# Kernel optimization log

Measured on AMD Instinct MI355X. Metric: run time of the kernel, lower is better.

## Reference

```python
import jax, jax.numpy as jnp
import numpy as np

N = 4096        # number_of_users
IN = 1000       # in_size (items)
H1, H2 = 2048, 1024
EMB = 512
HEADS = 8
OUT = 1000


def setup_inputs() -> dict:
    key = jax.random.key(0)
    ks = iter(jax.random.split(key, 32))
    def lin(i, o):
        return jax.random.normal(next(ks), (i, o), jnp.float32) * (1.0 / np.sqrt(i))
    inp = {"batch": jax.random.normal(next(ks), (N, IN), jnp.float32)}
    for p in ("q", "k", "v"):
        inp[p + "_w1"] = lin(IN, H1); inp[p + "_b1"] = jnp.zeros((H1,), jnp.float32)
        inp[p + "_w2"] = lin(H1, H2); inp[p + "_b2"] = jnp.zeros((H2,), jnp.float32)
        inp[p + "_w3"] = lin(H2, EMB); inp[p + "_b3"] = jnp.zeros((EMB,), jnp.float32)
    inp["wo_w"] = lin(EMB, OUT)
    inp["wo_b"] = jnp.zeros((OUT,), jnp.float32)
    return inp


def _mlp(x, w1, b1, w2, b2, w3, b3):
    h = jax.nn.relu(x @ w1 + b1)
    h = jax.nn.relu(h @ w2 + b2)
    return h @ w3 + b3


def _split_heads(x):
    # [N, EMB] -> [HEADS, N, depth]
    return x.reshape(N, HEADS, EMB // HEADS).transpose(1, 0, 2)


def reference(batch,
              q_w1, q_b1, q_w2, q_b2, q_w3, q_b3,
              k_w1, k_b1, k_w2, k_b2, k_w3, k_b3,
              v_w1, v_b1, v_w2, v_b2, v_w3, v_b3,
              wo_w, wo_b):
    q = _mlp(batch, q_w1, q_b1, q_w2, q_b2, q_w3, q_b3)
    k = _mlp(batch, k_w1, k_b1, k_w2, k_b2, k_w3, k_b3)
    v = _mlp(batch, v_w1, v_b1, v_w2, v_b2, v_w3, v_b3)
    qh = jax.nn.relu(_split_heads(q))
    kh = jax.nn.relu(_split_heads(k))
    vh = _split_heads(v)
    depth = EMB // HEADS
    # ReLU-normalized attention (no softmax): scores / row-sum
    scores = jnp.einsum('hnd,hmd->hnm', qh, kh) / jnp.sqrt(jnp.float32(depth))
    denom = jnp.sum(scores, axis=-1, keepdims=True) + 1e-8
    weights = scores / denom
    att = jnp.einsum('hnm,hmd->hnd', weights, vh)   # [H, N, depth]
    att = att.transpose(1, 0, 2).reshape(N, EMB)
    return att @ wo_w + wo_b
```

## Files before the change

### kernel.cpp

```cpp
#include <hip/hip_runtime.h>
#include <hip/hip_bf16.h>


typedef __attribute__((ext_vector_type(4))) float f32x4;
typedef __attribute__((ext_vector_type(4))) float float4v;
typedef __attribute__((ext_vector_type(8))) short bf16x8;

static constexpr size_t OFF_XB   = 0;
static constexpr size_t OFF_WT1  = OFF_XB   + 8388608;
static constexpr size_t OFF_WT2  = OFF_WT1  + 12582912;
static constexpr size_t OFF_WT3  = OFF_WT2  + 12582912;
static constexpr size_t OFF_MWT  = OFF_WT3  + 3145728;
static constexpr size_t OFF_B1C  = OFF_MWT  + 1048576;
static constexpr size_t OFF_H1   = OFF_B1C  + 24576;
static constexpr size_t OFF_H2   = OFF_H1   + 50331648;
static constexpr size_t OFF_QKV  = OFF_H2   + 25165824;
static constexpr size_t OFF_MP   = OFF_QKV  + 12582912;
static constexpr size_t OFF_MF   = OFF_MP   + 4259840;
static constexpr size_t OFF_QT   = OFF_MF   + 133120;

__device__ __forceinline__ void gload16(const __hip_bfloat16* g, __hip_bfloat16* l) {
  __builtin_amdgcn_global_load_lds(
      (const __attribute__((address_space(1))) void*)g,
      (__attribute__((address_space(3))) void*)l, 16, 0, 0);
}

__device__ __forceinline__ void xcd_map(int gx, int gy, int cm, int cn,
                                        int& zz, int& mt, int& nt) {
  const int gid = (blockIdx.z * gy + blockIdx.y) * gx + blockIdx.x;
  const int xcd = gid & 7;
  const int slot = gid >> 3;
  const int per = cm * cn;
  zz = slot / per;
  const int rem = slot % per;
  const int nxr = gx / cn;
  const int xr = xcd % nxr, yr = xcd / nxr;
  mt = yr * cm + rem % cm;
  nt = xr * cn + rem / cm;
}

__global__ __launch_bounds__(256) void prep(
    const float* __restrict__ w1a, const float* __restrict__ w1b, const float* __restrict__ w1c,
    const float* __restrict__ w2a, const float* __restrict__ w2b, const float* __restrict__ w2c,
    const float* __restrict__ w3a, const float* __restrict__ w3b, const float* __restrict__ w3c,
    const float* __restrict__ batch,
    __hip_bfloat16* __restrict__ WT1, __hip_bfloat16* __restrict__ WT2,
    __hip_bfloat16* __restrict__ WT3, __hip_bfloat16* __restrict__ XB) {
  const int b = blockIdx.x, t = threadIdx.x;
  if (b >= 3456) {
    int idx = (b - 3456) * 256 + t;
    int row = idx >> 8, c4 = (idx & 255) * 4;
    __hip_bfloat16 o[4];
    if (c4 < 1000) {
      float4v v = *reinterpret_cast<const float4v*>(&batch[(size_t)row * 1000 + c4]);
#pragma unroll
      for (int j = 0; j < 4; ++j) o[j] = __float2bfloat16(v[j]);
    } else {
#pragma unroll
      for (int j = 0; j < 4; ++j) o[j] = __float2bfloat16(0.f);
    }
    *reinterpret_cast<ushort4*>(&XB[(size_t)row * 1024 + c4]) =
        *reinterpret_cast<const ushort4*>(o);
    return;
  }
  __shared__ float tl[64][65];
  const float* in; __hip_bfloat16* out; int K, N, Kpad, kb, nb;
  if (b < 1536) {
    int mat = b / 512, r = b % 512;
    const float* s[3] = {w1a, w1b, w1c};
    in = s[mat]; out = WT1 + (size_t)mat * 2048 * 1024;
    K = 1000; N = 2048; Kpad = 1024; kb = r & 15; nb = r >> 4;
  } else if (b < 3072) {
    int r = b - 1536; int mat = r / 512; r %= 512;
    const float* s[3] = {w2a, w2b, w2c};
    in = s[mat]; out = WT2 + (size_t)mat * 1024 * 2048;
    K = 2048; N = 1024; Kpad = 2048; kb = r & 31; nb = r >> 5;
  } else {
    int r = b - 3072; int mat = r / 128; r %= 128;
    const float* s[3] = {w3a, w3b, w3c};
    in = s[mat]; out = WT3 + (size_t)mat * 512 * 1024;
    K = 1024; N = 512; Kpad = 1024; kb = r & 15; nb = r >> 4;
  }
  const int kb64 = kb * 64, nb64 = nb * 64;
  const int trow = t >> 4, tc4 = (t & 15) * 4;
#pragma unroll
  for (int it = 0; it < 4; ++it) {
    const int kl = it * 16 + trow;
    const int k = kb64 + kl;
    float4v v = {0.f, 0.f, 0.f, 0.f};
    if (k < K) v = *reinterpret_cast<const float4v*>(&in[(size_t)k * N + nb64 + tc4]);
    tl[kl][tc4 + 0] = v[0]; tl[kl][tc4 + 1] = v[1];
    tl[kl][tc4 + 2] = v[2]; tl[kl][tc4 + 3] = v[3];
  }
  __syncthreads();
  const int ln = t >> 2, ks = (t & 3) * 16;
  short ob[16];
#pragma unroll
  for (int u = 0; u < 16; ++u) {
    __hip_bfloat16 bb = __float2bfloat16(tl[ks + u][ln]);
    ob[u] = *(const short*)&bb;
  }
  __hip_bfloat16* dst = out + (size_t)(nb64 + ln) * Kpad + kb64 + ks;
  *reinterpret_cast<bf16x8*>(dst) = *reinterpret_cast<const bf16x8*>(&ob[0]);
  *reinterpret_cast<bf16x8*>(dst + 8) = *reinterpret_cast<const bf16x8*>(&ob[8]);
}

template <int NJ>
__global__ __launch_bounds__(256, 3) void gemm_fast(
    const __hip_bfloat16* __restrict__ A, int lda, size_t Az,
    const __hip_bfloat16* __restrict__ B, int ldb, size_t Bz,
    const float* __restrict__ bias0, const float* __restrict__ bias1,
    const float* __restrict__ bias2,
    void* __restrict__ Cout, int ldc, size_t Cz,
    int nlimit, int NT, int epi, int cm, int cn) {
  __shared__ __hip_bfloat16 smA[3][4096];
  __shared__ __hip_bfloat16 smB[3][NJ * 1024];
  const int t = threadIdx.x;
  int zz, mt, nt;
  xcd_map(gridDim.x, gridDim.y, cm, cn, zz, mt, nt);
  const int m0 = mt * 128, n0 = nt * (NJ * 32);
  A += (size_t)zz * Az;
  B += (size_t)zz * Bz;

  const int w = t >> 6, l = t & 63;
  const int wm = (w >> 1) * 64, wn = (w & 1) * (NJ * 16);
  const int fr = l & 15, fq = l >> 4;

  const int r0 = t >> 2;
  const int cg = (t & 3) ^ ((t >> 3) & 3);
  const __hip_bfloat16* gA0 = A + (size_t)(m0 + r0) * lda + cg * 8;
  const __hip_bfloat16* gA1 = gA0 + (size_t)64 * lda;
  const __hip_bfloat16* gB0 = B + (size_t)(n0 + r0) * ldb + cg * 8;
  const __hip_bfloat16* gB1 = gB0 + (size_t)64 * ldb;

  const int soff = (fq ^ ((fr >> 1) & 3)) * 8;
  int offA[4], offB[NJ];
#pragma unroll
  for (int i = 0; i < 4; ++i) offA[i] = (wm + i * 16 + fr) * 32 + soff;
#pragma unroll
  for (int j = 0; j < NJ; ++j) offB[j] = (wn + j * 16 + fr) * 32 + soff;

  f32x4 acc[4][NJ] = {};

#define STG(BUF, KT) do {                                                      \
    const size_t ko_ = (size_t)(KT) * 32;                                      \
    gload16(gA0 + ko_, &smA[BUF][w * 512]);                                    \
    gload16(gA1 + ko_, &smA[BUF][w * 512 + 2048]);                             \
    gload16(gB0 + ko_, &smB[BUF][w * 512]);                                    \
    if (NJ == 4) gload16(gB1 + ko_, &smB[BUF][w * 512 + 2048]);                \
  } while (0)

  STG(0, 0);
  STG(1, 1);

  int cur = 0;
  for (int T = 0; T < NT; ++T) {
    if (T == NT - 1)
      asm volatile("s_waitcnt vmcnt(0)" ::: "memory");
    else if (NJ == 4)
      asm volatile("s_waitcnt vmcnt(4)" ::: "memory");
    else
      asm volatile("s_waitcnt vmcnt(3)" ::: "memory");
    __builtin_amdgcn_s_barrier();
    __builtin_amdgcn_sched_barrier(0);
    bf16x8 af[4], bf[NJ];
#pragma unroll
    for (int i = 0; i < 4; ++i)
      af[i] = *reinterpret_cast<const bf16x8*>(&smA[cur][offA[i]]);
#pragma unroll
    for (int j = 0; j < NJ; ++j)
      bf[j] = *reinterpret_cast<const bf16x8*>(&smB[cur][offB[j]]);
    if (T + 2 < NT) {
      const int nb_ = (cur + 2 >= 3) ? cur - 1 : cur + 2;
      STG(nb_, T + 2);
    }
#pragma unroll
    for (int i = 0; i < 4; ++i)
#pragma unroll
      for (int j = 0; j < NJ; ++j)
        acc[i][j] = __builtin_amdgcn_mfma_f32_16x16x32_bf16(af[i], bf[j], acc[i][j], 0, 0, 0);
    cur = (cur + 1 >= 3) ? 0 : cur + 1;
  }
#undef STG

  const float* bz = (zz == 0) ? bias0 : ((zz == 1) ? bias1 : bias2);
  const bool dorelu = (epi == 1) || (epi == 4) || (epi == 3 && zz < 2);
  float bv[NJ];
#pragma unroll
  for (int j = 0; j < NJ; ++j) {
    const int col = n0 + wn + j * 16 + fr;
    if (epi == 4) {
      const float* bsel = (col < 2048) ? bias0 : ((col < 4096) ? bias1 : bias2);
      bv[j] = bsel[col & 2047];
    } else if (epi == 2) {
      bv[j] = (col < nlimit) ? bias0[col] : 0.f;
    } else {
      bv[j] = bz[col];
    }
  }
#pragma unroll
  for (int i = 0; i < 4; ++i) {
#pragma unroll
    for (int j = 0; j < NJ; ++j) {
      const int col = n0 + wn + j * 16 + fr;
#pragma unroll
      for (int rr = 0; rr < 4; ++rr) {
        const int row = m0 + wm + i * 16 + fq * 4 + rr;
        float v = acc[i][j][rr] + bv[j];
        if (dorelu) v = fmaxf(v, 0.f);
        if (epi == 2) {
          if (col < nlimit)
            ((float*)Cout)[(size_t)row * ldc + col] = v;
        } else {
          ((__hip_bfloat16*)Cout + (size_t)zz * Cz)[(size_t)row * ldc + col] =
              __float2bfloat16(v);
        }
      }
    }
  }
}

__global__ __launch_bounds__(256) void kv_outer(const __hip_bfloat16* __restrict__ QKV, int ld,
                                                float* __restrict__ part) {
  __shared__ __hip_bfloat16 kt[128][64];
  __shared__ __hip_bfloat16 vt[128][64];
  const int t = threadIdx.x;
  const int n0 = blockIdx.x * 128;
  const int h = blockIdx.y;
#pragma unroll
  for (int it = 0; it < 4; ++it) {
    int r = it * 32 + (t >> 3);
    int c = (t & 7) * 8;
    const __hip_bfloat16* kr = &QKV[(size_t)(n0 + r) * ld + 512 + h * 64 + c];
    const __hip_bfloat16* vr = &QKV[(size_t)(n0 + r) * ld + 1024 + h * 64 + c];
    *reinterpret_cast<bf16x8*>(&kt[r][c]) = *reinterpret_cast<const bf16x8*>(kr);
    *reinterpret_cast<bf16x8*>(&vt[r][c]) = *reinterpret_cast<const bf16x8*>(vr);
  }
  __syncthreads();
  const int i = t >> 2, j0 = (t & 3) << 4;
  float acc[16] = {};
  float ks = 0.f;
  for (int r = 0; r < 128; ++r) {
    float kv = __bfloat162float(kt[r][i]);
    ks += kv;
    bf16x8 va = *reinterpret_cast<const bf16x8*>(&vt[r][j0]);
    bf16x8 vb = *reinterpret_cast<const bf16x8*>(&vt[r][j0 + 8]);
#pragma unroll
    for (int jj = 0; jj < 8; ++jj) {
      ushort ua = (ushort)((const short*)&va)[jj];
      ushort ub = (ushort)((const short*)&vb)[jj];
      acc[jj]     += kv * __bfloat162float(*(const __hip_bfloat16*)&ua);
      acc[8 + jj] += kv * __bfloat162float(*(const __hip_bfloat16*)&ub);
    }
  }
  float* dst = part + ((size_t)blockIdx.x * 8 + h) * 4160;
#pragma unroll
  for (int jj = 0; jj < 16; ++jj) dst[i * 64 + j0 + jj] = acc[jj];
  if ((t & 3) == 0) dst[4096 + i] = ks;
}

__global__ __launch_bounds__(256) void reduce_m(const float* __restrict__ part,
                                                float* __restrict__ Mfin) {
  const int g = blockIdx.x * 256 + threadIdx.x;
  if (g >= 8 * 4160) return;
  const int h = g / 4160, idx = g % 4160;
  float s = 0.f;
#pragma unroll 4
  for (int c = 0; c < 32; ++c) s += part[((size_t)c * 8 + h) * 4160 + idx];
  Mfin[(size_t)h * 4160 + idx] = s;
}

__global__ __launch_bounds__(256) void mwq(const float* __restrict__ Mfin,
                                           const float* __restrict__ wo,
                                           __hip_bfloat16* __restrict__ MWT,
                                           const __hip_bfloat16* __restrict__ QKV,
                                           __hip_bfloat16* __restrict__ QT) {
  const int t = threadIdx.x;
  if (blockIdx.x < 32) {
    __shared__ float Ml[64][64];
    const int h = blockIdx.x >> 2;
    const int j = (blockIdx.x & 3) * 256 + t;
    const float* M = Mfin + (size_t)h * 4160;
    for (int e = t; e < 4096; e += 256)
      Ml[e >> 6][e & 63] = M[e];
    __syncthreads();
    float wcol[64];
    const bool valid = (j < 1000);
#pragma unroll
    for (int d = 0; d < 64; ++d)
      wcol[d] = valid ? wo[(size_t)(h * 64 + d) * 1000 + j] : 0.f;
    short ob[64];
#pragma unroll
    for (int i = 0; i < 64; ++i) {
      float a = 0.f;
#pragma unroll
      for (int d = 0; d < 64; ++d) a += Ml[i][d] * wcol[d];
      __hip_bfloat16 bb = __float2bfloat16(a);
      ob[i] = *(const short*)&bb;
    }
    __hip_bfloat16* dst = MWT + (size_t)j * 512 + h * 64;
#pragma unroll
    for (int v = 0; v < 8; ++v)
      *reinterpret_cast<bf16x8*>(dst + v * 8) = *reinterpret_cast<const bf16x8*>(&ob[v * 8]);
  } else {
    const int bid = blockIdx.x - 32;
    const int r = bid * 4 + (t >> 6);
    const int c = (t & 63) * 8;
    const int h = (t & 63) >> 3;
    bf16x8 qv = *reinterpret_cast<const bf16x8*>(&QKV[(size_t)r * 1536 + c]);
    float qf[8];
#pragma unroll
    for (int j = 0; j < 8; ++j) {
      ushort u = (ushort)((const short*)&qv)[j];
      qf[j] = __bfloat162float(*(const __hip_bfloat16*)&u);
    }
    const float* ks = Mfin + (size_t)h * 4160 + 4096 + (c & 63);
    float s = 0.f;
#pragma unroll
    for (int j = 0; j < 8; ++j) s += qf[j] * ks[j];
    s += __shfl_xor(s, 1, 8);
    s += __shfl_xor(s, 2, 8);
    s += __shfl_xor(s, 4, 8);
    const float inv = 0.125f / (s * 0.125f + 1e-8f);
    bf16x8 o;
#pragma unroll
    for (int j = 0; j < 8; ++j) {
      __hip_bfloat16 bb = __float2bfloat16(qf[j] * inv);
      ((short*)&o)[j] = *(const short*)&bb;
    }
    *reinterpret_cast<bf16x8*>(&QT[(size_t)r * 512 + c]) = o;
  }
}

extern "C" void kernel_launch(void* const* d_in, const int* in_sizes, int n_in,
                              void* d_out, int out_size, void* d_ws, size_t ws_size,
                              hipStream_t stream) {
  const float* batch = (const float*)d_in[0];
  const float* w1[3] = {(const float*)d_in[1],  (const float*)d_in[7],  (const float*)d_in[13]};
  const float* b1[3] = {(const float*)d_in[2],  (const float*)d_in[8],  (const float*)d_in[14]};
  const float* w2[3] = {(const float*)d_in[3],  (const float*)d_in[9],  (const float*)d_in[15]};
  const float* b2[3] = {(const float*)d_in[4],  (const float*)d_in[10], (const float*)d_in[16]};
  const float* w3[3] = {(const float*)d_in[5],  (const float*)d_in[11], (const float*)d_in[17]};
  const float* b3[3] = {(const float*)d_in[6],  (const float*)d_in[12], (const float*)d_in[18]};
  const float* wow   = (const float*)d_in[19];
  const float* wob   = (const float*)d_in[20];

  char* ws = (char*)d_ws;
  __hip_bfloat16* XB  = (__hip_bfloat16*)(ws + OFF_XB);
  __hip_bfloat16* WT1 = (__hip_bfloat16*)(ws + OFF_WT1);
  __hip_bfloat16* WT2 = (__hip_bfloat16*)(ws + OFF_WT2);
  __hip_bfloat16* WT3 = (__hip_bfloat16*)(ws + OFF_WT3);
  __hip_bfloat16* MWT = (__hip_bfloat16*)(ws + OFF_MWT);
  __hip_bfloat16* H1  = (__hip_bfloat16*)(ws + OFF_H1);
  __hip_bfloat16* H2  = (__hip_bfloat16*)(ws + OFF_H2);
  __hip_bfloat16* QKV = (__hip_bfloat16*)(ws + OFF_QKV);
  float*          MP  = (float*)(ws + OFF_MP);
  float*          MF  = (float*)(ws + OFF_MF);
  __hip_bfloat16* QT  = (__hip_bfloat16*)(ws + OFF_QT);
  float*          OUT = (float*)d_out;

  prep<<<7552, 256, 0, stream>>>(w1[0], w1[1], w1[2], w2[0], w2[1], w2[2],
                                 w3[0], w3[1], w3[2], batch, WT1, WT2, WT3, XB);

  gemm_fast<4><<<dim3(48, 32, 1), 256, 0, stream>>>(
      XB, 1024, 0, WT1, 1024, 0, b1[0], b1[1], b1[2], H1, 6144, 0,
      6144, 32, 4, 16, 12);
  gemm_fast<4><<<dim3(8, 32, 3), 256, 0, stream>>>(
      H1, 6144, 2048, WT2, 2048, (size_t)1024 * 2048,
      b2[0], b2[1], b2[2], H2, 3072, 1024, 1024, 64, 1, 8, 4);
  gemm_fast<2><<<dim3(8, 32, 3), 256, 0, stream>>>(
      H2, 3072, 1024, WT3, 1024, (size_t)512 * 1024,
      b3[0], b3[1], b3[2], QKV, 1536, 512, 512, 32, 3, 8, 4);

  kv_outer<<<dim3(32, 8), 256, 0, stream>>>(QKV, 1536, MP);
  reduce_m<<<130, 256, 0, stream>>>(MP, MF);
  mwq<<<1056, 256, 0, stream>>>(MF, wow, MWT, QKV, QT);

  gemm_fast<2><<<dim3(16, 32, 1), 256, 0, stream>>>(
      QT, 512, 0, MWT, 512, 0, wob, wob, wob, OUT, 1000, 0,
      1000, 16, 2, 16, 4);

  (void)in_sizes; (void)n_in; (void)out_size; (void)ws_size;
}
```

Measured before the change: 237.9 us.

## Load GEMM A fragments directly from global into registers, bypass LDS

The GEMM kernel no longer stages the A tile through shared memory. Each wave now reads its A MFMA fragments straight from global memory into registers, double-buffered across a main loop unrolled by two. Only B still goes through the LDS triple buffer. This cuts LDS traffic and capacity use, but the A loads become strided 16-byte reads duplicated across the two waves sharing the same rows. Each step now waits for vmcnt(0), which may expose global latency where the old code kept prefetches in flight.

```diff
diff --git a/kernel.cpp b/kernel.cpp
--- a/kernel.cpp
+++ b/kernel.cpp
@@ -106,14 +106,13 @@
 }
 
 template <int NJ>
-__global__ __launch_bounds__(256, 3) void gemm_fast(
+__global__ __launch_bounds__(256, 3) void gemm_ar(
     const __hip_bfloat16* __restrict__ A, int lda, size_t Az,
     const __hip_bfloat16* __restrict__ B, int ldb, size_t Bz,
     const float* __restrict__ bias0, const float* __restrict__ bias1,
     const float* __restrict__ bias2,
     void* __restrict__ Cout, int ldc, size_t Cz,
     int nlimit, int NT, int epi, int cm, int cn) {
-  __shared__ __hip_bfloat16 smA[3][4096];
   __shared__ __hip_bfloat16 smB[3][NJ * 1024];
   const int t = threadIdx.x;
   int zz, mt, nt;
@@ -128,60 +127,75 @@
 
   const int r0 = t >> 2;
   const int cg = (t & 3) ^ ((t >> 3) & 3);
-  const __hip_bfloat16* gA0 = A + (size_t)(m0 + r0) * lda + cg * 8;
-  const __hip_bfloat16* gA1 = gA0 + (size_t)64 * lda;
   const __hip_bfloat16* gB0 = B + (size_t)(n0 + r0) * ldb + cg * 8;
   const __hip_bfloat16* gB1 = gB0 + (size_t)64 * ldb;
 
   const int soff = (fq ^ ((fr >> 1) & 3)) * 8;
-  int offA[4], offB[NJ];
-#pragma unroll
-  for (int i = 0; i < 4; ++i) offA[i] = (wm + i * 16 + fr) * 32 + soff;
+  int offB[NJ];
 #pragma unroll
   for (int j = 0; j < NJ; ++j) offB[j] = (wn + j * 16 + fr) * 32 + soff;
 
+  const __hip_bfloat16* aP[4];
+#pragma unroll
+  for (int i = 0; i < 4; ++i)
+    aP[i] = A + (size_t)(m0 + wm + i * 16 + fr) * lda + fq * 8;
+
   f32x4 acc[4][NJ] = {};
-
-#define STG(BUF, KT) do {                                                      \
+  bf16x8 afA[4], afB[4];
+
+#define STGB(BUF, KT) do {                                                     \
     const size_t ko_ = (size_t)(KT) * 32;                                      \
-    gload16(gA0 + ko_, &smA[BUF][w * 512]);                                    \
-    gload16(gA1 + ko_, &smA[BUF][w * 512 + 2048]);                             \
     gload16(gB0 + ko_, &smB[BUF][w * 512]);                                    \
     if (NJ == 4) gload16(gB1 + ko_, &smB[BUF][w * 512 + 2048]);                \
   } while (0)
 
-  STG(0, 0);
-  STG(1, 1);
+#define LOADA(DST, KT) do {                                                    \
+    _Pragma("unroll") for (int i_ = 0; i_ < 4; ++i_)                           \
+      DST[i_] = *reinterpret_cast<const bf16x8*>(aP[i_] + (size_t)(KT) * 32);  \
+  } while (0)
+
+#define MM(AF, BF) do {                                                        \
+    _Pragma("unroll") for (int i_ = 0; i_ < 4; ++i_)                           \
+      _Pragma("unroll") for (int j_ = 0; j_ < NJ; ++j_)                        \
+        acc[i_][j_] = __builtin_amdgcn_mfma_f32_16x16x32_bf16(                 \
+            AF[i_], BF[j_], acc[i_][j_], 0, 0, 0);                             \
+  } while (0)
+
+  LOADA(afA, 0);
+  STGB(0, 0);
+  STGB(1, 1);
 
   int cur = 0;
-  for (int T = 0; T < NT; ++T) {
-    if (T == NT - 1)
-      asm volatile("s_waitcnt vmcnt(0)" ::: "memory");
-    else if (NJ == 4)
-      asm volatile("s_waitcnt vmcnt(4)" ::: "memory");
-    else
-      asm volatile("s_waitcnt vmcnt(3)" ::: "memory");
+  for (int TT = 0; TT < NT; TT += 2) {
+    const int b1 = (cur + 1 >= 3) ? cur - 2 : cur + 1;
+    const int b2 = (cur + 2 >= 3) ? cur - 1 : cur + 2;
+    asm volatile("s_waitcnt vmcnt(0)" ::: "memory");
     __builtin_amdgcn_s_barrier();
     __builtin_amdgcn_sched_barrier(0);
-    bf16x8 af[4], bf[NJ];
-#pragma unroll
-    for (int i = 0; i < 4; ++i)
-      af[i] = *reinterpret_cast<const bf16x8*>(&smA[cur][offA[i]]);
+    bf16x8 bfa[NJ];
 #pragma unroll
     for (int j = 0; j < NJ; ++j)
-      bf[j] = *reinterpret_cast<const bf16x8*>(&smB[cur][offB[j]]);
-    if (T + 2 < NT) {
-      const int nb_ = (cur + 2 >= 3) ? cur - 1 : cur + 2;
-      STG(nb_, T + 2);
-    }
-#pragma unroll
-    for (int i = 0; i < 4; ++i)
+      bfa[j] = *reinterpret_cast<const bf16x8*>(&smB[cur][offB[j]]);
+    if (TT + 2 < NT) STGB(b2, TT + 2);
+    if (TT + 1 < NT) LOADA(afB, TT + 1);
+    MM(afA, bfa);
+    if (TT + 1 < NT) {
+      asm volatile("s_waitcnt vmcnt(0)" ::: "memory");
+      __builtin_amdgcn_s_barrier();
+      __builtin_amdgcn_sched_barrier(0);
+      bf16x8 bfb[NJ];
 #pragma unroll
       for (int j = 0; j < NJ; ++j)
-        acc[i][j] = __builtin_amdgcn_mfma_f32_16x16x32_bf16(af[i], bf[j], acc[i][j], 0, 0, 0);
-    cur = (cur + 1 >= 3) ? 0 : cur + 1;
-  }
-#undef STG
+        bfb[j] = *reinterpret_cast<const bf16x8*>(&smB[b1][offB[j]]);
+      if (TT + 3 < NT) STGB(cur, TT + 3);
+      if (TT + 2 < NT) LOADA(afA, TT + 2);
+      MM(afB, bfb);
+    }
+    cur = (cur + 2 >= 3) ? cur - 1 : cur + 2;
+  }
+#undef STGB
+#undef LOADA
+#undef MM
 
   const float* bz = (zz == 0) ? bias0 : ((zz == 1) ? bias1 : bias2);
   const bool dorelu = (epi == 1) || (epi == 4) || (epi == 3 && zz < 2);
@@ -362,13 +376,13 @@
   prep<<<7552, 256, 0, stream>>>(w1[0], w1[1], w1[2], w2[0], w2[1], w2[2],
                                  w3[0], w3[1], w3[2], batch, WT1, WT2, WT3, XB);
 
-  gemm_fast<4><<<dim3(48, 32, 1), 256, 0, stream>>>(
+  gemm_ar<4><<<dim3(48, 32, 1), 256, 0, stream>>>(
       XB, 1024, 0, WT1, 1024, 0, b1[0], b1[1], b1[2], H1, 6144, 0,
       6144, 32, 4, 16, 12);
-  gemm_fast<4><<<dim3(8, 32, 3), 256, 0, stream>>>(
+  gemm_ar<4><<<dim3(8, 32, 3), 256, 0, stream>>>(
       H1, 6144, 2048, WT2, 2048, (size_t)1024 * 2048,
       b2[0], b2[1], b2[2], H2, 3072, 1024, 1024, 64, 1, 8, 4);
-  gemm_fast<2><<<dim3(8, 32, 3), 256, 0, stream>>>(
+  gemm_ar<2><<<dim3(8, 32, 3), 256, 0, stream>>>(
       H2, 3072, 1024, WT3, 1024, (size_t)512 * 1024,
       b3[0], b3[1], b3[2], QKV, 1536, 512, 512, 32, 3, 8, 4);
 
@@ -376,7 +390,7 @@
   reduce_m<<<130, 256, 0, stream>>>(MP, MF);
   mwq<<<1056, 256, 0, stream>>>(MF, wow, MWT, QKV, QT);
 
-  gemm_fast<2><<<dim3(16, 32, 1), 256, 0, stream>>>(
+  gemm_ar<2><<<dim3(16, 32, 1), 256, 0, stream>>>(
       QT, 512, 0, MWT, 512, 0, wob, wob, wob, OUT, 1000, 0,
       1000, 16, 2, 16, 4);
 
```

Measured after the change: 374.4 us. 57.4% more time.
